# Optimization experiments

Hardware: AMD Instinct MI355X
Metric: run time of the kernel (lower is better)

Reference implementation:

```python
import jax, jax.numpy as jnp
import numpy as np
from jax.ops import segment_sum, segment_max

N_NODES = 10000
N_EDGES = 160000
N_GRAPHS = 32
IN_DIM = 128
HID = 256
HEADS = 4


def setup_inputs() -> dict:
    key = jax.random.key(0)
    ks = jax.random.split(key, 12)
    x = jax.random.normal(ks[0], (N_NODES, IN_DIM), dtype=jnp.float32)
    edge_index = jax.random.randint(ks[1], (2, N_EDGES), 0, N_NODES, dtype=jnp.int64)
    batch = jnp.sort(jax.random.randint(ks[2], (N_NODES,), 0, N_GRAPHS, dtype=jnp.int64))
    s = 0.05
    params = {
        "W1": jax.random.normal(ks[3], (IN_DIM, HID), dtype=jnp.float32) * s,
        "b1": jnp.zeros((HID,), dtype=jnp.float32),
        "W2": jax.random.normal(ks[4], (HID, HID), dtype=jnp.float32) * s,
        "b2": jnp.zeros((HID,), dtype=jnp.float32),
        "Wg": jax.random.normal(ks[5], (HID, HEADS * HID), dtype=jnp.float32) * s,
        "att_src": jax.random.normal(ks[6], (HEADS, HID), dtype=jnp.float32) * s,
        "att_dst": jax.random.normal(ks[7], (HEADS, HID), dtype=jnp.float32) * s,
        "bg": jnp.zeros((HID,), dtype=jnp.float32),
        "W_heads": jax.random.normal(ks[8], (HID, 4), dtype=jnp.float32) * s,
        "b_heads": jnp.zeros((4,), dtype=jnp.float32),
    }
    return {"x": x, "edge_index": edge_index, "batch": batch, **params}


def _add_self_loops(edge_index, n):
    loop = jnp.arange(n, dtype=edge_index.dtype)
    src = jnp.concatenate([edge_index[0], loop])
    dst = jnp.concatenate([edge_index[1], loop])
    return src, dst


def _gcn_conv(x, W, b, src, dst, n):
    # PyG GCNConv: add self-loops, symmetric normalization D^-1/2 A D^-1/2
    h = x @ W                                   # [N, out]
    deg = segment_sum(jnp.ones_like(src, dtype=h.dtype), dst, num_segments=n)
    dinv = jax.lax.rsqrt(jnp.maximum(deg, 1e-12))
    coef = dinv[src] * dinv[dst]                # [E+N]
    out = segment_sum(h[src] * coef[:, None], dst, num_segments=n)
    return out + b


def _gat_conv(x, Wg, att_src, att_dst, bg, src, dst, n):
    # PyG GATConv(heads=4, concat=False): mean over heads, leaky_relu slope 0.2
    h = (x @ Wg).reshape(n, HEADS, HID)         # [N, H, C]
    a_src = jnp.einsum('nhc,hc->nh', h, att_src)
    a_dst = jnp.einsum('nhc,hc->nh', h, att_dst)
    e = jax.nn.leaky_relu(a_src[src] + a_dst[dst], 0.2)   # [E+N, H]
    m = segment_max(e, dst, num_segments=n)
    e = jnp.exp(e - m[dst])
    z = segment_sum(e, dst, num_segments=n)
    alpha = e / (z[dst] + 1e-16)                # softmax over edges into each dst
    out = segment_sum(h[src] * alpha[:, :, None], dst, num_segments=n)  # [N, H, C]
    return out.mean(axis=1) + bg


def reference(x, edge_index, batch, W1, b1, W2, b2, Wg, att_src, att_dst, bg, W_heads, b_heads):
    n = x.shape[0]
    src, dst = _add_self_loops(edge_index, n)
    h1 = jax.nn.relu(_gcn_conv(x, W1, b1, src, dst, n))
    h2 = jax.nn.relu(_gcn_conv(h1, W2, b2, src, dst, n))
    h3 = jax.nn.relu(_gat_conv(h2, Wg, att_src, att_dst, bg, src, dst, n))
    # global_mean_pool
    ones = jnp.ones((n,), dtype=h3.dtype)
    cnt = segment_sum(ones, batch, num_segments=N_GRAPHS)
    pooled = segment_sum(h3, batch, num_segments=N_GRAPHS) / jnp.maximum(cnt, 1.0)[:, None]
    # four scalar heads stacked: cols = [energy_absorption, elastic_modulus, ballistic_limit, penetration_resistance]
    return pooled @ W_heads + b_heads           # [G, 4]
```

## Files before the change

### kernel.cpp

```cpp
#include <hip/hip_runtime.h>
#include <cmath>

#define IN_DIM 128
#define HID 256
#define NHEADS 4
#define NGRAPHS 32

typedef unsigned short u16;
typedef __attribute__((ext_vector_type(8))) short bfrag8;
typedef __attribute__((ext_vector_type(4))) float f32x4;

__device__ __forceinline__ u16 f2bf(float x) {
  unsigned u = __float_as_uint(x);
  unsigned r = (u + 0x7fffu + ((u >> 16) & 1u)) >> 16;
  return (u16)r;
}
__device__ __forceinline__ float bf2f(u16 v) {
  return __uint_as_float(((unsigned)v) << 16);
}
__device__ __forceinline__ float lof(unsigned u) { return __uint_as_float(u << 16); }
__device__ __forceinline__ float hif(unsigned u) { return __uint_as_float(u & 0xffff0000u); }
__device__ __forceinline__ float lrelu02(float x) { return x > 0.f ? x : 0.2f * x; }

#define GACC(U, W)                                                   \
  acc[0] += (W) * lof((U).x); acc[1] += (W) * hif((U).x);            \
  acc[2] += (W) * lof((U).y); acc[3] += (W) * hif((U).y);            \
  acc[4] += (W) * lof((U).z); acc[5] += (W) * hif((U).z);            \
  acc[6] += (W) * lof((U).w); acc[7] += (W) * hif((U).w);

#define GACC2(U, W)                                                  \
  a0 += (W) * lof((U).x); a1 += (W) * hif((U).x);                    \
  a2 += (W) * lof((U).y); a3 += (W) * hif((U).y);

__global__ __launch_bounds__(256) void count_edges_k(const int* __restrict__ dst,
                                                     int* __restrict__ cnt, int E) {
  int i = blockIdx.x * 256 + threadIdx.x;
  if (i < E) atomicAdd(&cnt[dst[i]], 1);
}

__global__ __launch_bounds__(256) void fill_csr_k(const int* __restrict__ src,
                                                  const int* __restrict__ dst,
                                                  const int* __restrict__ row_ptr,
                                                  int* __restrict__ cursor,
                                                  int* __restrict__ csr_src, int E) {
  int i = blockIdx.x * 256 + threadIdx.x;
  if (i < E) {
    int d = dst[i];
    int p = atomicAdd(&cursor[d], 1);
    csr_src[row_ptr[d] + p] = src[i];
  }
}

__device__ void scan_dev(const int* __restrict__ cnt, int* __restrict__ row_ptr,
                         float* __restrict__ dinv, int n) {
  __shared__ int s_w[4];
  __shared__ int s_off[4];
  __shared__ int s_tot;
  int tid = threadIdx.x, wv = tid >> 6, lane = tid & 63;
  int carry = 0;
  int nch = (n + 255) >> 8;
  for (int c = 0; c < nch; c++) {
    int i = (c << 8) + tid;
    int v = (i < n) ? cnt[i] : 0;
    int incl = v;
    #pragma unroll
    for (int off = 1; off < 64; off <<= 1) {
      int t = __shfl_up(incl, off);
      if (lane >= off) incl += t;
    }
    if (lane == 63) s_w[wv] = incl;
    __syncthreads();
    if (tid == 0) {
      int a0 = s_w[0], a1 = s_w[1], a2 = s_w[2], a3 = s_w[3];
      s_off[0] = 0; s_off[1] = a0; s_off[2] = a0 + a1; s_off[3] = a0 + a1 + a2;
      s_tot = a0 + a1 + a2 + a3;
    }
    __syncthreads();
    int excl = incl - v + s_off[wv] + carry;
    if (i < n) {
      row_ptr[i] = excl;
      dinv[i] = rsqrtf((float)(v + 1));
    }
    carry += s_tot;
    __syncthreads();
  }
  if (tid == 0) row_ptr[n] = carry;
}

__device__ void pack_a_dev(const float* __restrict__ A, u16* __restrict__ Ap,
                           int K, int KT, int wid, int lane) {
  int fm = wid / KT, kt = wid - fm * KT;
  int m = fm * 16 + (lane & 15);
  int kb = kt * 32 + (lane >> 4) * 8;
  const float* src = A + (size_t)m * K + kb;
  float4 v0 = *(const float4*)src;
  float4 v1 = *(const float4*)(src + 4);
  float vv[8] = {v0.x, v0.y, v0.z, v0.w, v1.x, v1.y, v1.z, v1.w};
  u16 hi[8], lo[8];
  #pragma unroll
  for (int j = 0; j < 8; j++) {
    u16 h = f2bf(vv[j]);
    hi[j] = h;
    lo[j] = f2bf(vv[j] - bf2f(h));
  }
  u16* dstp = Ap + ((size_t)fm * KT + kt) * 1024 + lane * 8;
  *(ushort4*)(dstp)       = make_ushort4(hi[0], hi[1], hi[2], hi[3]);
  *(ushort4*)(dstp + 4)   = make_ushort4(hi[4], hi[5], hi[6], hi[7]);
  *(ushort4*)(dstp + 512) = make_ushort4(lo[0], lo[1], lo[2], lo[3]);
  *(ushort4*)(dstp + 516) = make_ushort4(lo[4], lo[5], lo[6], lo[7]);
}

__device__ void pack_b_dev(const float* __restrict__ B, u16* __restrict__ Bp,
                           int N, int KT, int wid, int lane) {
  int fn = wid / KT, kt = wid - fn * KT;
  int n = fn * 16 + (lane & 15);
  int kb = kt * 32 + (lane >> 4) * 8;
  float vv[8];
  #pragma unroll
  for (int j = 0; j < 8; j++) vv[j] = B[(size_t)(kb + j) * N + n];
  u16 hi[8], lo[8];
  #pragma unroll
  for (int j = 0; j < 8; j++) {
    u16 h = f2bf(vv[j]);
    hi[j] = h;
    lo[j] = f2bf(vv[j] - bf2f(h));
  }
  u16* dstp = Bp + ((size_t)fn * KT + kt) * 1024 + lane * 8;
  *(ushort4*)(dstp)       = make_ushort4(hi[0], hi[1], hi[2], hi[3]);
  *(ushort4*)(dstp + 4)   = make_ushort4(hi[4], hi[5], hi[6], hi[7]);
  *(ushort4*)(dstp + 512) = make_ushort4(lo[0], lo[1], lo[2], lo[3]);
  *(ushort4*)(dstp + 516) = make_ushort4(lo[4], lo[5], lo[6], lo[7]);
}

__global__ __launch_bounds__(256) void prep_k(const float* __restrict__ x,
                                              const float* __restrict__ W1,
                                              const float* __restrict__ W2,
                                              const float* __restrict__ Wg,
                                              const float* __restrict__ att_src,
                                              const float* __restrict__ att_dst,
                                              const int* __restrict__ cnt,
                                              int* __restrict__ row_ptr,
                                              float* __restrict__ dinv,
                                              u16* __restrict__ xp,
                                              u16* __restrict__ w1p,
                                              u16* __restrict__ w2p,
                                              u16* __restrict__ wgp,
                                              float* __restrict__ w_s,
                                              float* __restrict__ w_d,
                                              int NFM, int N) {
  __shared__ float red_s[4][NHEADS];
  __shared__ float red_d[4][NHEADS];
  int b = blockIdx.x;
  int tid = threadIdx.x;
  int lane = tid & 63;
  if (b == 0) {
    scan_dev(cnt, row_ptr, dinv, N);
    return;
  }
  b -= 1;
  int XB = NFM;
  if (b < XB) {
    int wid = b * 4 + (tid >> 6);
    if (wid < NFM * 4) pack_a_dev(x, xp, IN_DIM, 4, wid, lane);
  } else if (b < XB + 16) {
    pack_b_dev(W1, w1p, HID, 4, (b - XB) * 4 + (tid >> 6), lane);
  } else if (b < XB + 48) {
    pack_b_dev(W2, w2p, HID, 8, (b - XB - 16) * 4 + (tid >> 6), lane);
  } else if (b < XB + 176) {
    pack_b_dev(Wg, wgp, NHEADS * HID, 8, (b - XB - 48) * 4 + (tid >> 6), lane);
  } else {
    int k = b - (XB + 176);
    int c = tid, wvv = c >> 6, ln = c & 63;
    #pragma unroll
    for (int h = 0; h < NHEADS; h++) {
      float w = Wg[(size_t)k * (NHEADS * HID) + h * HID + c];
      float vs = w * att_src[h * HID + c];
      float vd = w * att_dst[h * HID + c];
      #pragma unroll
      for (int off = 32; off; off >>= 1) {
        vs += __shfl_xor(vs, off);
        vd += __shfl_xor(vd, off);
      }
      if (ln == 0) { red_s[wvv][h] = vs; red_d[wvv][h] = vd; }
    }
    __syncthreads();
    if (c < NHEADS)
      w_s[k * NHEADS + c] = red_s[0][c] + red_s[1][c] + red_s[2][c] + red_s[3][c];
    else if (c < 2 * NHEADS) {
      int h = c - NHEADS;
      w_d[k * NHEADS + h] = red_d[0][h] + red_d[1][h] + red_d[2][h] + red_d[3][h];
    }
  }
}

template <int KT, int LDC, bool ALO>
__global__ __launch_bounds__(256) void mfma_gemm_k(const u16* __restrict__ Ap,
                                                   const u16* __restrict__ Bp,
                                                   u16* __restrict__ Cb, int M) {
  int tid = threadIdx.x;
  int w = tid >> 6, lane = tid & 63;
  int wm = w >> 1, wn = w & 1;
  int fm0 = blockIdx.y * 4 + wm * 2;
  int fn0 = blockIdx.x * 4 + wn * 2;
  f32x4 acc[2][2] = {};
  #pragma unroll
  for (int kt = 0; kt < KT; kt++) {
    bfrag8 a_hi[2], a_lo[2], b_hi[2], b_lo[2];
    #pragma unroll
    for (int f = 0; f < 2; f++) {
      const u16* pa = Ap + ((size_t)(fm0 + f) * KT + kt) * 1024 + lane * 8;
      a_hi[f] = *(const bfrag8*)pa;
      if constexpr (ALO) a_lo[f] = *(const bfrag8*)(pa + 512);
      const u16* pb = Bp + ((size_t)(fn0 + f) * KT + kt) * 1024 + lane * 8;
      b_hi[f] = *(const bfrag8*)pb;
      b_lo[f] = *(const bfrag8*)(pb + 512);
    }
    #pragma unroll
    for (int f = 0; f < 2; f++) {
      #pragma unroll
      for (int g = 0; g < 2; g++) {
        acc[f][g] = __builtin_amdgcn_mfma_f32_16x16x32_bf16(a_hi[f], b_hi[g], acc[f][g], 0, 0, 0);
        acc[f][g] = __builtin_amdgcn_mfma_f32_16x16x32_bf16(a_hi[f], b_lo[g], acc[f][g], 0, 0, 0);
        if constexpr (ALO)
          acc[f][g] = __builtin_amdgcn_mfma_f32_16x16x32_bf16(a_lo[f], b_hi[g], acc[f][g], 0, 0, 0);
      }
    }
  }
  int r0 = (lane >> 4) * 4;
  int cl = lane & 15;
  #pragma unroll
  for (int f = 0; f < 2; f++) {
    #pragma unroll
    for (int g = 0; g < 2; g++) {
      int col = (fn0 + g) * 16 + cl;
      #pragma unroll
      for (int r = 0; r < 4; r++) {
        int row = (fm0 + f) * 16 + r0 + r;
        if (row < M) Cb[(size_t)row * LDC + col] = f2bf(acc[f][g][r]);
      }
    }
  }
}

template <bool LOGITS, bool PACK_LO, bool SORT>
__global__ __launch_bounds__(256) void gcn_agg_k(const u16* __restrict__ t,
                                                 const int* __restrict__ row_ptr,
                                                 int* __restrict__ csr_src,
                                                 const float* __restrict__ dinv,
                                                 const float* __restrict__ bias,
                                                 u16* __restrict__ apack,
                                                 const float* __restrict__ w_s,
                                                 const float* __restrict__ w_d,
                                                 float4* __restrict__ a_src4,
                                                 float4* __restrict__ a_dst4, int N) {
  int wv = threadIdx.x >> 6, lane = threadIdx.x & 63;
  int i = blockIdx.x * 4 + wv;
  if (i >= N) return;
  float di = dinv[i];
  int c4 = lane * 4;
  int beg = row_ptr[i], end = row_ptr[i + 1];
  int deg = end - beg;
  float a0, a1, a2, a3;
  {
    uint2 u = *(const uint2*)&t[(size_t)i * HID + c4];
    float w = di * di;
    a0 = w * lof(u.x); a1 = w * hif(u.x); a2 = w * lof(u.y); a3 = w * hif(u.y);
  }
  if (deg <= 64) {
    int s = (lane < deg) ? csr_src[beg + lane] : 0x7fffffff;
    if constexpr (SORT) {
      if (deg > 1) {
        #pragma unroll
        for (int k = 2; k <= 64; k <<= 1) {
          #pragma unroll
          for (int j = k >> 1; j > 0; j >>= 1) {
            int vp = __shfl_xor(s, j);
            bool lower = ((lane & j) == 0);
            bool up = ((lane & k) == 0);
            int mn = min(s, vp), mx = max(s, vp);
            s = (lower == up) ? mn : mx;
          }
        }
        if (lane < deg) csr_src[beg + lane] = s;
      }
    }
    float w = (lane < deg) ? dinv[s] * di : 0.f;
    int e = 0;
    for (; e + 3 < deg; e += 4) {
      int s0 = __shfl(s, e), s1 = __shfl(s, e + 1);
      int s2 = __shfl(s, e + 2), s3 = __shfl(s, e + 3);
      float w0 = __shfl(w, e), w1 = __shfl(w, e + 1);
      float w2 = __shfl(w, e + 2), w3 = __shfl(w, e + 3);
      uint2 u0 = *(const uint2*)&t[(size_t)s0 * HID + c4];
      uint2 u1 = *(const uint2*)&t[(size_t)s1 * HID + c4];
      uint2 u2 = *(const uint2*)&t[(size_t)s2 * HID + c4];
      uint2 u3 = *(const uint2*)&t[(size_t)s3 * HID + c4];
      GACC2(u0, w0); GACC2(u1, w1); GACC2(u2, w2); GACC2(u3, w3);
    }
    for (; e < deg; e++) {
      int s0 = __shfl(s, e);
      float w0 = __shfl(w, e);
      uint2 u = *(const uint2*)&t[(size_t)s0 * HID + c4];
      GACC2(u, w0);
    }
  } else {
    int e = beg;
    for (; e + 3 < end; e += 4) {
      int s0 = csr_src[e + 0], s1 = csr_src[e + 1];
      int s2 = csr_src[e + 2], s3 = csr_src[e + 3];
      float w0 = dinv[s0] * di, w1 = dinv[s1] * di;
      float w2 = dinv[s2] * di, w3 = dinv[s3] * di;
      uint2 u0 = *(const uint2*)&t[(size_t)s0 * HID + c4];
      uint2 u1 = *(const uint2*)&t[(size_t)s1 * HID + c4];
      uint2 u2 = *(const uint2*)&t[(size_t)s2 * HID + c4];
      uint2 u3 = *(const uint2*)&t[(size_t)s3 * HID + c4];
      GACC2(u0, w0); GACC2(u1, w1); GACC2(u2, w2); GACC2(u3, w3);
    }
    for (; e < end; e++) {
      int s = csr_src[e];
      float w = dinv[s] * di;
      uint2 u = *(const uint2*)&t[(size_t)s * HID + c4];
      GACC2(u, w);
    }
  }
  float4 bv = *(const float4*)&bias[c4];
  float v0 = fmaxf(a0 + bv.x, 0.f), v1 = fmaxf(a1 + bv.y, 0.f);
  float v2 = fmaxf(a2 + bv.z, 0.f), v3 = fmaxf(a3 + bv.w, 0.f);
  {
    int fm = i >> 4, kt = c4 >> 5;
    int pl = (i & 15) + 16 * ((c4 >> 3) & 3);
    int j = c4 & 7;
    size_t base = ((size_t)fm * 8 + kt) * 1024 + pl * 8 + j;
    u16 h0 = f2bf(v0), h1 = f2bf(v1), h2 = f2bf(v2), h3 = f2bf(v3);
    *(ushort4*)&apack[base] = make_ushort4(h0, h1, h2, h3);
    if constexpr (PACK_LO)
      *(ushort4*)&apack[base + 512] =
          make_ushort4(f2bf(v0 - bf2f(h0)), f2bf(v1 - bf2f(h1)),
                       f2bf(v2 - bf2f(h2)), f2bf(v3 - bf2f(h3)));
  }
  if constexpr (LOGITS) {
    const float4* ws4 = (const float4*)w_s;
    const float4* wd4 = (const float4*)w_d;
    float4 s0 = ws4[c4 + 0], s1 = ws4[c4 + 1], s2 = ws4[c4 + 2], s3 = ws4[c4 + 3];
    float4 d0 = wd4[c4 + 0], d1 = wd4[c4 + 1], d2 = wd4[c4 + 2], d3 = wd4[c4 + 3];
    float ps0 = v0 * s0.x + v1 * s1.x + v2 * s2.x + v3 * s3.x;
    float ps1 = v0 * s0.y + v1 * s1.y + v2 * s2.y + v3 * s3.y;
    float ps2 = v0 * s0.z + v1 * s1.z + v2 * s2.z + v3 * s3.z;
    float ps3 = v0 * s0.w + v1 * s1.w + v2 * s2.w + v3 * s3.w;
    float pd0 = v0 * d0.x + v1 * d1.x + v2 * d2.x + v3 * d3.x;
    float pd1 = v0 * d0.y + v1 * d1.y + v2 * d2.y + v3 * d3.y;
    float pd2 = v0 * d0.z + v1 * d1.z + v2 * d2.z + v3 * d3.z;
    float pd3 = v0 * d0.w + v1 * d1.w + v2 * d2.w + v3 * d3.w;
    #pragma unroll
    for (int off = 32; off; off >>= 1) {
      ps0 += __shfl_xor(ps0, off); ps1 += __shfl_xor(ps1, off);
      ps2 += __shfl_xor(ps2, off); ps3 += __shfl_xor(ps3, off);
      pd0 += __shfl_xor(pd0, off); pd1 += __shfl_xor(pd1, off);
      pd2 += __shfl_xor(pd2, off); pd3 += __shfl_xor(pd3, off);
    }
    if (lane == 0) {
      a_src4[i] = make_float4(ps0, ps1, ps2, ps3);
      a_dst4[i] = make_float4(pd0, pd1, pd2, pd3);
    }
  }
}

__global__ __launch_bounds__(256) void gat_agg_k(const u16* __restrict__ hgT,
                                                 const int* __restrict__ row_ptr,
                                                 const int* __restrict__ csr_src,
                                                 const float4* __restrict__ a_src4,
                                                 const float4* __restrict__ a_dst4,
                                                 const float* __restrict__ bg,
                                                 float* __restrict__ out, int N) {
  __shared__ int s_src[4][64];
  __shared__ float s_al[4][2][64];
  __shared__ float s_comb[2][32][9];
  int wv = threadIdx.x >> 6, lane = threadIdx.x & 63;
  int nodeSlot = wv >> 1, half = wv & 1;
  int i = blockIdx.x * 2 + nodeSlot;
  if (i >= N) { __syncthreads(); return; }
  int beg = row_ptr[i], end = row_ptr[i + 1];
  int deg = end - beg;
  float4 ad = a_dst4[i];
  int hsel = lane >> 5;
  const u16* rowbase = hgT + half * 512 + lane * 8;
  float acc[8];
  #pragma unroll
  for (int j = 0; j < 8; j++) acc[j] = 0.f;

  if (deg <= 63) {
    int s = (lane < deg) ? csr_src[beg + lane] : i;
    bool valid = (lane <= deg);
    float4 as = a_src4[s];
    float l0 = valid ? lrelu02(as.x + ad.x) : -INFINITY;
    float l1 = valid ? lrelu02(as.y + ad.y) : -INFINITY;
    float l2 = valid ? lrelu02(as.z + ad.z) : -INFINITY;
    float l3 = valid ? lrelu02(as.w + ad.w) : -INFINITY;
    float m0 = l0, m1 = l1, m2 = l2, m3 = l3;
    #pragma unroll
    for (int off = 32; off; off >>= 1) {
      m0 = fmaxf(m0, __shfl_xor(m0, off)); m1 = fmaxf(m1, __shfl_xor(m1, off));
      m2 = fmaxf(m2, __shfl_xor(m2, off)); m3 = fmaxf(m3, __shfl_xor(m3, off));
    }
    float e0 = valid ? expf(l0 - m0) : 0.f;
    float e1 = valid ? expf(l1 - m1) : 0.f;
    float e2 = valid ? expf(l2 - m2) : 0.f;
    float e3 = valid ? expf(l3 - m3) : 0.f;
    float z0 = e0, z1 = e1, z2 = e2, z3 = e3;
    #pragma unroll
    for (int off = 32; off; off >>= 1) {
      z0 += __shfl_xor(z0, off); z1 += __shfl_xor(z1, off);
      z2 += __shfl_xor(z2, off); z3 += __shfl_xor(z3, off);
    }
    s_src[wv][lane] = s;
    if (half == 0) {
      s_al[wv][0][lane] = e0 / (z0 + 1e-16f);
      s_al[wv][1][lane] = e1 / (z1 + 1e-16f);
    } else {
      s_al[wv][0][lane] = e2 / (z2 + 1e-16f);
      s_al[wv][1][lane] = e3 / (z3 + 1e-16f);
    }
    int nk = deg + 1;
    int e = 0;
    for (; e + 3 < nk; e += 4) {
      int sa = s_src[wv][e + 0], sb = s_src[wv][e + 1];
      int sc = s_src[wv][e + 2], sd = s_src[wv][e + 3];
      float wa = s_al[wv][hsel][e + 0], wb = s_al[wv][hsel][e + 1];
      float wc = s_al[wv][hsel][e + 2], wd = s_al[wv][hsel][e + 3];
      uint4 ua = *(const uint4*)(rowbase + (size_t)sa * 1024);
      uint4 ub = *(const uint4*)(rowbase + (size_t)sb * 1024);
      uint4 uc = *(const uint4*)(rowbase + (size_t)sc * 1024);
      uint4 ud = *(const uint4*)(rowbase + (size_t)sd * 1024);
      GACC(ua, wa); GACC(ub, wb); GACC(uc, wc); GACC(ud, wd);
    }
    for (; e < nk; e++) {
      int sa = s_src[wv][e];
      float wa = s_al[wv][hsel][e];
      uint4 ua = *(const uint4*)(rowbase + (size_t)sa * 1024);
      GACC(ua, wa);
    }
  } else {
    float4 asi = a_src4[i];
    float ls0 = lrelu02(asi.x + ad.x), ls1 = lrelu02(asi.y + ad.y);
    float ls2 = lrelu02(asi.z + ad.z), ls3 = lrelu02(asi.w + ad.w);
    float m0 = ls0, m1 = ls1, m2 = ls2, m3 = ls3;
    for (int e = beg + lane; e < end; e += 64) {
      float4 as = a_src4[csr_src[e]];
      m0 = fmaxf(m0, lrelu02(as.x + ad.x)); m1 = fmaxf(m1, lrelu02(as.y + ad.y));
      m2 = fmaxf(m2, lrelu02(as.z + ad.z)); m3 = fmaxf(m3, lrelu02(as.w + ad.w));
    }
    #pragma unroll
    for (int off = 32; off; off >>= 1) {
      m0 = fmaxf(m0, __shfl_xor(m0, off)); m1 = fmaxf(m1, __shfl_xor(m1, off));
      m2 = fmaxf(m2, __shfl_xor(m2, off)); m3 = fmaxf(m3, __shfl_xor(m3, off));
    }
    float z0 = (lane == 0) ? expf(ls0 - m0) : 0.f;
    float z1 = (lane == 0) ? expf(ls1 - m1) : 0.f;
    float z2 = (lane == 0) ? expf(ls2 - m2) : 0.f;
    float z3 = (lane == 0) ? expf(ls3 - m3) : 0.f;
    for (int e = beg + lane; e < end; e += 64) {
      float4 as = a_src4[csr_src[e]];
      z0 += expf(lrelu02(as.x + ad.x) - m0); z1 += expf(lrelu02(as.y + ad.y) - m1);
      z2 += expf(lrelu02(as.z + ad.z) - m2); z3 += expf(lrelu02(as.w + ad.w) - m3);
    }
    #pragma unroll
    for (int off = 32; off; off >>= 1) {
      z0 += __shfl_xor(z0, off); z1 += __shfl_xor(z1, off);
      z2 += __shfl_xor(z2, off); z3 += __shfl_xor(z3, off);
    }
    float iz0 = 1.f / (z0 + 1e-16f), iz1 = 1.f / (z1 + 1e-16f);
    float iz2 = 1.f / (z2 + 1e-16f), iz3 = 1.f / (z3 + 1e-16f);
    {
      float w0 = expf(ls0 - m0) * iz0, w1 = expf(ls1 - m1) * iz1;
      float w2 = expf(ls2 - m2) * iz2, w3 = expf(ls3 - m3) * iz3;
      float aw = (half == 0) ? (hsel == 0 ? w0 : w1) : (hsel == 0 ? w2 : w3);
      uint4 u = *(const uint4*)(rowbase + (size_t)i * 1024);
      GACC(u, aw);
    }
    for (int base = beg; base < end; base += 64) {
      int mc = min(64, end - base);
      if (lane < mc) {
        int s = csr_src[base + lane];
        float4 as = a_src4[s];
        s_src[wv][lane] = s;
        if (half == 0) {
          s_al[wv][0][lane] = expf(lrelu02(as.x + ad.x) - m0) * iz0;
          s_al[wv][1][lane] = expf(lrelu02(as.y + ad.y) - m1) * iz1;
        } else {
          s_al[wv][0][lane] = expf(lrelu02(as.z + ad.z) - m2) * iz2;
          s_al[wv][1][lane] = expf(lrelu02(as.w + ad.w) - m3) * iz3;
        }
      }
      for (int e = 0; e < mc; e++) {
        int sa = s_src[wv][e];
        float wa = s_al[wv][hsel][e];
        uint4 ua = *(const uint4*)(rowbase + (size_t)sa * 1024);
        GACC(ua, wa);
      }
    }
  }
  #pragma unroll
  for (int j = 0; j < 8; j++) acc[j] += __shfl_xor(acc[j], 32);
  if (half == 1 && lane < 32) {
    #pragma unroll
    for (int j = 0; j < 8; j++) s_comb[nodeSlot][lane][j] = acc[j];
  }
  __syncthreads();
  if (half == 0 && lane < 32) {
    int cb = lane * 8;
    float o[8];
    #pragma unroll
    for (int j = 0; j < 8; j++)
      o[j] = fmaxf((acc[j] + s_comb[nodeSlot][lane][j]) * 0.25f + bg[cb + j], 0.f);
    float* op = out + (size_t)i * HID + cb;
    *(float4*)(op + 0) = make_float4(o[0], o[1], o[2], o[3]);
    *(float4*)(op + 4) = make_float4(o[4], o[5], o[6], o[7]);
  }
}

#define POOL_CHUNK 50
__global__ __launch_bounds__(256) void pool_acc_k(const float* __restrict__ h3,
                                                  const int* __restrict__ batch,
                                                  float* __restrict__ pooled,
                                                  float* __restrict__ gcnt, int N) {
  int c = threadIdx.x;
  int i0 = blockIdx.x * POOL_CHUNK;
  int i1 = min(i0 + POOL_CHUNK, N);
  if (i0 >= N) return;
  float acc = 0.f;
  int cur = batch[i0];
  int cnt_local = 0;
  for (int i = i0; i < i1; i++) {
    int g = batch[i];
    if (g != cur) {
      atomicAdd(&pooled[cur * HID + c], acc);
      if (c == 0) atomicAdd(&gcnt[cur], (float)cnt_local);
      acc = 0.f;
      cnt_local = 0;
      cur = g;
    }
    acc += h3[(size_t)i * HID + c];
    cnt_local++;
  }
  atomicAdd(&pooled[cur * HID + c], acc);
  if (c == 0) atomicAdd(&gcnt[cur], (float)cnt_local);
}

__global__ __launch_bounds__(128) void head_k(const float* __restrict__ pooled,
                                              const float* __restrict__ gcnt,
                                              const float* __restrict__ W_heads,
                                              const float* __restrict__ b_heads,
                                              float* __restrict__ out) {
  int tid = threadIdx.x;
  if (tid >= NGRAPHS * 4) return;
  int g = tid >> 2, k = tid & 3;
  float invc = 1.f / fmaxf(gcnt[g], 1.f);
  float acc = 0.f;
  for (int c = 0; c < HID; c++) acc += pooled[g * HID + c] * W_heads[c * 4 + k];
  out[g * 4 + k] = acc * invc + b_heads[k];
}

extern "C" void kernel_launch(void* const* d_in, const int* in_sizes, int n_in,
                              void* d_out, int out_size, void* d_ws, size_t ws_size,
                              hipStream_t stream) {
  const float* x = (const float*)d_in[0];
  const int* ei = (const int*)d_in[1];
  const int* batch = (const int*)d_in[2];
  const float* W1 = (const float*)d_in[3];
  const float* b1 = (const float*)d_in[4];
  const float* W2 = (const float*)d_in[5];
  const float* b2 = (const float*)d_in[6];
  const float* Wg = (const float*)d_in[7];
  const float* att_src = (const float*)d_in[8];
  const float* att_dst = (const float*)d_in[9];
  const float* bg = (const float*)d_in[10];
  const float* W_heads = (const float*)d_in[11];
  const float* b_heads = (const float*)d_in[12];
  float* out = (float*)d_out;

  const int N = in_sizes[0] / IN_DIM;
  const int E = in_sizes[1] / 2;
  const int* src = ei;
  const int* dst = ei + E;

  const int NFM = N / 16;
  const int NFMP = ((N + 63) / 64) * 4;

  char* ws = (char*)d_ws;
  size_t off = 0;
  auto take = [&](size_t bytes) -> char* {
    char* p = ws + off;
    off = (off + bytes + 255) & ~(size_t)255;
    return p;
  };
  int* cnt      = (int*)take((size_t)N * 4);
  int* cursor   = (int*)take((size_t)N * 4);
  float* pooled = (float*)take((size_t)NGRAPHS * HID * 4 + NGRAPHS * 4);
  float* gcnt   = pooled + NGRAPHS * HID;
  size_t zero_span = off;
  int* row_ptr  = (int*)take((size_t)(N + 1) * 4);
  int* csr_src  = (int*)take((size_t)E * 4);
  float* dinv   = (float*)take((size_t)N * 4);
  float4* a_src4 = (float4*)take((size_t)N * 16);
  float4* a_dst4 = (float4*)take((size_t)N * 16);
  float* w_s    = (float*)take((size_t)HID * NHEADS * 4);
  float* w_d    = (float*)take((size_t)HID * NHEADS * 4);
  u16*   tb     = (u16*)take((size_t)N * HID * 2);
  float* h3     = (float*)take((size_t)N * HID * 4);
  u16*   hgT    = (u16*)take((size_t)N * NHEADS * HID * 2);
  u16*   xp     = (u16*)take((size_t)NFMP * 4 * 1024 * 2);
  u16*   h1p    = (u16*)take((size_t)NFMP * 8 * 1024 * 2);
  u16*   h2p    = (u16*)take((size_t)NFMP * 8 * 1024 * 2);
  u16*   w1p    = (u16*)take((size_t)16 * 4 * 1024 * 2);
  u16*   w2p    = (u16*)take((size_t)16 * 8 * 1024 * 2);
  u16*   wgp    = (u16*)take((size_t)64 * 8 * 1024 * 2);

  hipMemsetAsync(cnt, 0, zero_span, stream);

  int eb = (E + 255) / 256;
  count_edges_k<<<eb, 256, 0, stream>>>(dst, cnt, E);
  prep_k<<<1 + NFM + 176 + 256, 256, 0, stream>>>(x, W1, W2, Wg, att_src, att_dst,
                                                  cnt, row_ptr, dinv,
                                                  xp, w1p, w2p, wgp, w_s, w_d, NFM, N);
  fill_csr_k<<<eb, 256, 0, stream>>>(src, dst, row_ptr, cursor, csr_src, E);

  int mg64 = (N + 63) / 64;
  int ng4 = (N + 3) / 4;
  int ng2 = (N + 1) / 2;
  mfma_gemm_k<4, HID, true><<<dim3(4, mg64), 256, 0, stream>>>(xp, w1p, tb, N);
  gcn_agg_k<false, true, true><<<ng4, 256, 0, stream>>>(tb, row_ptr, csr_src, dinv, b1,
                                                        h1p, nullptr, nullptr, nullptr, nullptr, N);
  mfma_gemm_k<8, HID, true><<<dim3(4, mg64), 256, 0, stream>>>(h1p, w2p, tb, N);
  gcn_agg_k<true, false, false><<<ng4, 256, 0, stream>>>(tb, row_ptr, csr_src, dinv, b2,
                                                         h2p, w_s, w_d, a_src4, a_dst4, N);
  mfma_gemm_k<8, NHEADS * HID, false><<<dim3(16, mg64), 256, 0, stream>>>(h2p, wgp, hgT, N);
  gat_agg_k<<<ng2, 256, 0, stream>>>(hgT, row_ptr, csr_src, a_src4, a_dst4, bg, h3, N);
  int pb = (N + POOL_CHUNK - 1) / POOL_CHUNK;
  pool_acc_k<<<pb, 256, 0, stream>>>(h3, batch, pooled, gcnt, N);
  head_k<<<1, 128, 0, stream>>>(pooled, gcnt, W_heads, b_heads, out);
}
```

Before: 205.2 us.

## Remap GEMM blocks per XCD, drop in-kernel neighbor sort, widen GAT gather unroll

The GEMM launch becomes a 1D grid whose block ids are remapped so that all column tiles of a row tile land on the same XCD, improving L2 reuse of A rows. The bitonic sort of each node's neighbor list in the first GCN aggregation is removed, which saves shuffles and a write-back but gives up the locality that sorted gathers had. The GAT aggregation gather loop is unrolled to 8 outstanding 16-byte loads to raise memory-level parallelism at the cost of more registers.

```diff
diff --git a/kernel.cpp b/kernel.cpp
--- a/kernel.cpp
+++ b/kernel.cpp
@@ -193,15 +193,22 @@
   }
 }
 
-template <int KT, int LDC, bool ALO>
+template <int KT, int LDC, bool ALO, int GX>
 __global__ __launch_bounds__(256) void mfma_gemm_k(const u16* __restrict__ Ap,
                                                    const u16* __restrict__ Bp,
-                                                   u16* __restrict__ Cb, int M) {
+                                                   u16* __restrict__ Cb,
+                                                   int M, int MY) {
+  int bid = blockIdx.x;
+  int xcd = bid & 7;
+  int j = bid >> 3;
+  int by = xcd + 8 * (j / GX);
+  int bx = j - (j / GX) * GX;
+  if (by >= MY) return;
   int tid = threadIdx.x;
   int w = tid >> 6, lane = tid & 63;
   int wm = w >> 1, wn = w & 1;
-  int fm0 = blockIdx.y * 4 + wm * 2;
-  int fn0 = blockIdx.x * 4 + wn * 2;
+  int fm0 = by * 4 + wm * 2;
+  int fn0 = bx * 4 + wn * 2;
   f32x4 acc[2][2] = {};
   #pragma unroll
   for (int kt = 0; kt < KT; kt++) {
@@ -242,10 +249,10 @@
   }
 }
 
-template <bool LOGITS, bool PACK_LO, bool SORT>
+template <bool LOGITS, bool PACK_LO>
 __global__ __launch_bounds__(256) void gcn_agg_k(const u16* __restrict__ t,
                                                  const int* __restrict__ row_ptr,
-                                                 int* __restrict__ csr_src,
+                                                 const int* __restrict__ csr_src,
                                                  const float* __restrict__ dinv,
                                                  const float* __restrict__ bias,
                                                  u16* __restrict__ apack,
@@ -267,23 +274,7 @@
     a0 = w * lof(u.x); a1 = w * hif(u.x); a2 = w * lof(u.y); a3 = w * hif(u.y);
   }
   if (deg <= 64) {
-    int s = (lane < deg) ? csr_src[beg + lane] : 0x7fffffff;
-    if constexpr (SORT) {
-      if (deg > 1) {
-        #pragma unroll
-        for (int k = 2; k <= 64; k <<= 1) {
-          #pragma unroll
-          for (int j = k >> 1; j > 0; j >>= 1) {
-            int vp = __shfl_xor(s, j);
-            bool lower = ((lane & j) == 0);
-            bool up = ((lane & k) == 0);
-            int mn = min(s, vp), mx = max(s, vp);
-            s = (lower == up) ? mn : mx;
-          }
-        }
-        if (lane < deg) csr_src[beg + lane] = s;
-      }
-    }
+    int s = (lane < deg) ? csr_src[beg + lane] : 0;
     float w = (lane < deg) ? dinv[s] * di : 0.f;
     int e = 0;
     for (; e + 3 < deg; e += 4) {
@@ -422,16 +413,20 @@
     }
     int nk = deg + 1;
     int e = 0;
-    for (; e + 3 < nk; e += 4) {
-      int sa = s_src[wv][e + 0], sb = s_src[wv][e + 1];
-      int sc = s_src[wv][e + 2], sd = s_src[wv][e + 3];
-      float wa = s_al[wv][hsel][e + 0], wb = s_al[wv][hsel][e + 1];
-      float wc = s_al[wv][hsel][e + 2], wd = s_al[wv][hsel][e + 3];
-      uint4 ua = *(const uint4*)(rowbase + (size_t)sa * 1024);
-      uint4 ub = *(const uint4*)(rowbase + (size_t)sb * 1024);
-      uint4 uc = *(const uint4*)(rowbase + (size_t)sc * 1024);
-      uint4 ud = *(const uint4*)(rowbase + (size_t)sd * 1024);
-      GACC(ua, wa); GACC(ub, wb); GACC(uc, wc); GACC(ud, wd);
+    for (; e + 7 < nk; e += 8) {
+      int sv[8];
+      float wvv[8];
+      #pragma unroll
+      for (int q = 0; q < 8; q++) {
+        sv[q] = s_src[wv][e + q];
+        wvv[q] = s_al[wv][hsel][e + q];
+      }
+      uint4 u[8];
+      #pragma unroll
+      for (int q = 0; q < 8; q++)
+        u[q] = *(const uint4*)(rowbase + (size_t)sv[q] * 1024);
+      #pragma unroll
+      for (int q = 0; q < 8; q++) { GACC(u[q], wvv[q]); }
     }
     for (; e < nk; e++) {
       int sa = s_src[wv][e];
@@ -624,16 +619,18 @@
                                                   xp, w1p, w2p, wgp, w_s, w_d, NFM, N);
   fill_csr_k<<<eb, 256, 0, stream>>>(src, dst, row_ptr, cursor, csr_src, E);
 
-  int mg64 = (N + 63) / 64;
+  const int MY = (N + 63) / 64;
+  const int gemm_blks4 = 8 * ((MY + 7) / 8) * 4;
+  const int gemm_blks16 = 8 * ((MY + 7) / 8) * 16;
   int ng4 = (N + 3) / 4;
   int ng2 = (N + 1) / 2;
-  mfma_gemm_k<4, HID, true><<<dim3(4, mg64), 256, 0, stream>>>(xp, w1p, tb, N);
-  gcn_agg_k<false, true, true><<<ng4, 256, 0, stream>>>(tb, row_ptr, csr_src, dinv, b1,
-                                                        h1p, nullptr, nullptr, nullptr, nullptr, N);
-  mfma_gemm_k<8, HID, true><<<dim3(4, mg64), 256, 0, stream>>>(h1p, w2p, tb, N);
-  gcn_agg_k<true, false, false><<<ng4, 256, 0, stream>>>(tb, row_ptr, csr_src, dinv, b2,
-                                                         h2p, w_s, w_d, a_src4, a_dst4, N);
-  mfma_gemm_k<8, NHEADS * HID, false><<<dim3(16, mg64), 256, 0, stream>>>(h2p, wgp, hgT, N);
+  mfma_gemm_k<4, HID, true, 4><<<gemm_blks4, 256, 0, stream>>>(xp, w1p, tb, N, MY);
+  gcn_agg_k<false, true><<<ng4, 256, 0, stream>>>(tb, row_ptr, csr_src, dinv, b1,
+                                                  h1p, nullptr, nullptr, nullptr, nullptr, N);
+  mfma_gemm_k<8, HID, true, 4><<<gemm_blks4, 256, 0, stream>>>(h1p, w2p, tb, N, MY);
+  gcn_agg_k<true, false><<<ng4, 256, 0, stream>>>(tb, row_ptr, csr_src, dinv, b2,
+                                                  h2p, w_s, w_d, a_src4, a_dst4, N);
+  mfma_gemm_k<8, NHEADS * HID, false, 16><<<gemm_blks16, 256, 0, stream>>>(h2p, wgp, hgT, N, MY);
   gat_agg_k<<<ng2, 256, 0, stream>>>(hgT, row_ptr, csr_src, a_src4, a_dst4, bg, h3, N);
   int pb = (N + POOL_CHUNK - 1) / POOL_CHUNK;
   pool_acc_k<<<pb, 256, 0, stream>>>(h3, batch, pooled, gcnt, N);
```

Measured after the change: 210.9 us. 2.8% more time.

## Fuse mean-pool with regression heads and drop in-wave CSR sort

Applied to the files above, without the earlier changes.

Global mean pooling and the four regression heads are merged into one kernel. Each block binary-searches its graph's node range in the sorted batch array, sums one strided part of the rows, and applies W_heads before atomically adding into the zeroed output. This removes a launch and the pooled scratch buffer, at the cost of an extra memset of the output. Separately, the GCN aggregation loses its shuffle-based small-degree path and the bitonic sort of CSR sources, so neighbour order stays as fill_csr produced it and gather locality may get worse.

```diff
diff --git a/kernel.cpp b/kernel.cpp
--- a/kernel.cpp
+++ b/kernel.cpp
@@ -242,10 +242,10 @@
   }
 }
 
-template <bool LOGITS, bool PACK_LO, bool SORT>
+template <bool LOGITS, bool PACK_LO>
 __global__ __launch_bounds__(256) void gcn_agg_k(const u16* __restrict__ t,
                                                  const int* __restrict__ row_ptr,
-                                                 int* __restrict__ csr_src,
+                                                 const int* __restrict__ csr_src,
                                                  const float* __restrict__ dinv,
                                                  const float* __restrict__ bias,
                                                  u16* __restrict__ apack,
@@ -259,69 +259,29 @@
   float di = dinv[i];
   int c4 = lane * 4;
   int beg = row_ptr[i], end = row_ptr[i + 1];
-  int deg = end - beg;
   float a0, a1, a2, a3;
   {
     uint2 u = *(const uint2*)&t[(size_t)i * HID + c4];
     float w = di * di;
     a0 = w * lof(u.x); a1 = w * hif(u.x); a2 = w * lof(u.y); a3 = w * hif(u.y);
   }
-  if (deg <= 64) {
-    int s = (lane < deg) ? csr_src[beg + lane] : 0x7fffffff;
-    if constexpr (SORT) {
-      if (deg > 1) {
-        #pragma unroll
-        for (int k = 2; k <= 64; k <<= 1) {
-          #pragma unroll
-          for (int j = k >> 1; j > 0; j >>= 1) {
-            int vp = __shfl_xor(s, j);
-            bool lower = ((lane & j) == 0);
-            bool up = ((lane & k) == 0);
-            int mn = min(s, vp), mx = max(s, vp);
-            s = (lower == up) ? mn : mx;
-          }
-        }
-        if (lane < deg) csr_src[beg + lane] = s;
-      }
-    }
-    float w = (lane < deg) ? dinv[s] * di : 0.f;
-    int e = 0;
-    for (; e + 3 < deg; e += 4) {
-      int s0 = __shfl(s, e), s1 = __shfl(s, e + 1);
-      int s2 = __shfl(s, e + 2), s3 = __shfl(s, e + 3);
-      float w0 = __shfl(w, e), w1 = __shfl(w, e + 1);
-      float w2 = __shfl(w, e + 2), w3 = __shfl(w, e + 3);
-      uint2 u0 = *(const uint2*)&t[(size_t)s0 * HID + c4];
-      uint2 u1 = *(const uint2*)&t[(size_t)s1 * HID + c4];
-      uint2 u2 = *(const uint2*)&t[(size_t)s2 * HID + c4];
-      uint2 u3 = *(const uint2*)&t[(size_t)s3 * HID + c4];
-      GACC2(u0, w0); GACC2(u1, w1); GACC2(u2, w2); GACC2(u3, w3);
-    }
-    for (; e < deg; e++) {
-      int s0 = __shfl(s, e);
-      float w0 = __shfl(w, e);
-      uint2 u = *(const uint2*)&t[(size_t)s0 * HID + c4];
-      GACC2(u, w0);
-    }
-  } else {
-    int e = beg;
-    for (; e + 3 < end; e += 4) {
-      int s0 = csr_src[e + 0], s1 = csr_src[e + 1];
-      int s2 = csr_src[e + 2], s3 = csr_src[e + 3];
-      float w0 = dinv[s0] * di, w1 = dinv[s1] * di;
-      float w2 = dinv[s2] * di, w3 = dinv[s3] * di;
-      uint2 u0 = *(const uint2*)&t[(size_t)s0 * HID + c4];
-      uint2 u1 = *(const uint2*)&t[(size_t)s1 * HID + c4];
-      uint2 u2 = *(const uint2*)&t[(size_t)s2 * HID + c4];
-      uint2 u3 = *(const uint2*)&t[(size_t)s3 * HID + c4];
-      GACC2(u0, w0); GACC2(u1, w1); GACC2(u2, w2); GACC2(u3, w3);
-    }
-    for (; e < end; e++) {
-      int s = csr_src[e];
-      float w = dinv[s] * di;
-      uint2 u = *(const uint2*)&t[(size_t)s * HID + c4];
-      GACC2(u, w);
-    }
+  int e = beg;
+  for (; e + 3 < end; e += 4) {
+    int s0 = csr_src[e + 0], s1 = csr_src[e + 1];
+    int s2 = csr_src[e + 2], s3 = csr_src[e + 3];
+    float w0 = dinv[s0] * di, w1 = dinv[s1] * di;
+    float w2 = dinv[s2] * di, w3 = dinv[s3] * di;
+    uint2 u0 = *(const uint2*)&t[(size_t)s0 * HID + c4];
+    uint2 u1 = *(const uint2*)&t[(size_t)s1 * HID + c4];
+    uint2 u2 = *(const uint2*)&t[(size_t)s2 * HID + c4];
+    uint2 u3 = *(const uint2*)&t[(size_t)s3 * HID + c4];
+    GACC2(u0, w0); GACC2(u1, w1); GACC2(u2, w2); GACC2(u3, w3);
+  }
+  for (; e < end; e++) {
+    int s = csr_src[e];
+    float w = dinv[s] * di;
+    uint2 u = *(const uint2*)&t[(size_t)s * HID + c4];
+    GACC2(u, w);
   }
   float4 bv = *(const float4*)&bias[c4];
   float v0 = fmaxf(a0 + bv.x, 0.f), v1 = fmaxf(a1 + bv.y, 0.f);
@@ -518,46 +478,50 @@
   }
 }
 
-#define POOL_CHUNK 50
-__global__ __launch_bounds__(256) void pool_acc_k(const float* __restrict__ h3,
-                                                  const int* __restrict__ batch,
-                                                  float* __restrict__ pooled,
-                                                  float* __restrict__ gcnt, int N) {
+__global__ __launch_bounds__(256) void pool_head_k(const float* __restrict__ h3,
+                                                   const int* __restrict__ batch,
+                                                   const float* __restrict__ W_heads,
+                                                   const float* __restrict__ b_heads,
+                                                   float* __restrict__ out, int N) {
+  int g = blockIdx.x >> 3;
+  int part = blockIdx.x & 7;
   int c = threadIdx.x;
-  int i0 = blockIdx.x * POOL_CHUNK;
-  int i1 = min(i0 + POOL_CHUNK, N);
-  if (i0 >= N) return;
-  float acc = 0.f;
-  int cur = batch[i0];
-  int cnt_local = 0;
-  for (int i = i0; i < i1; i++) {
-    int g = batch[i];
-    if (g != cur) {
-      atomicAdd(&pooled[cur * HID + c], acc);
-      if (c == 0) atomicAdd(&gcnt[cur], (float)cnt_local);
-      acc = 0.f;
-      cnt_local = 0;
-      cur = g;
-    }
-    acc += h3[(size_t)i * HID + c];
-    cnt_local++;
-  }
-  atomicAdd(&pooled[cur * HID + c], acc);
-  if (c == 0) atomicAdd(&gcnt[cur], (float)cnt_local);
-}
-
-__global__ __launch_bounds__(128) void head_k(const float* __restrict__ pooled,
-                                              const float* __restrict__ gcnt,
-                                              const float* __restrict__ W_heads,
-                                              const float* __restrict__ b_heads,
-                                              float* __restrict__ out) {
-  int tid = threadIdx.x;
-  if (tid >= NGRAPHS * 4) return;
-  int g = tid >> 2, k = tid & 3;
-  float invc = 1.f / fmaxf(gcnt[g], 1.f);
-  float acc = 0.f;
-  for (int c = 0; c < HID; c++) acc += pooled[g * HID + c] * W_heads[c * 4 + k];
-  out[g * 4 + k] = acc * invc + b_heads[k];
+  __shared__ int s_bounds[2];
+  if (c < 2) {
+    int target = g + c;
+    int lo = 0, hi = N;
+    while (lo < hi) {
+      int mid = (lo + hi) >> 1;
+      if (batch[mid] < target) lo = mid + 1; else hi = mid;
+    }
+    s_bounds[c] = lo;
+  }
+  __syncthreads();
+  int i0 = s_bounds[0], i1 = s_bounds[1];
+  float acc0 = 0.f, acc1 = 0.f;
+  int i = i0 + part;
+  for (; i + 8 < i1; i += 16) {
+    acc0 += h3[(size_t)i * HID + c];
+    acc1 += h3[(size_t)(i + 8) * HID + c];
+  }
+  if (i < i1) acc0 += h3[(size_t)i * HID + c];
+  float acc = acc0 + acc1;
+  float invc = 1.f / fmaxf((float)(i1 - i0), 1.f);
+  float4 wh = *(const float4*)&W_heads[c * 4];
+  float p0 = acc * wh.x, p1 = acc * wh.y, p2 = acc * wh.z, p3 = acc * wh.w;
+  int lane = c & 63, wv = c >> 6;
+  #pragma unroll
+  for (int off = 32; off; off >>= 1) {
+    p0 += __shfl_xor(p0, off); p1 += __shfl_xor(p1, off);
+    p2 += __shfl_xor(p2, off); p3 += __shfl_xor(p3, off);
+  }
+  __shared__ float s_red[4][4];
+  if (lane == 0) { s_red[wv][0] = p0; s_red[wv][1] = p1; s_red[wv][2] = p2; s_red[wv][3] = p3; }
+  __syncthreads();
+  if (c < 4) {
+    float r = s_red[0][c] + s_red[1][c] + s_red[2][c] + s_red[3][c];
+    atomicAdd(&out[g * 4 + c], r * invc + b_heads[c] * 0.125f);
+  }
 }
 
 extern "C" void kernel_launch(void* const* d_in, const int* in_sizes, int n_in,
@@ -595,8 +559,6 @@
   };
   int* cnt      = (int*)take((size_t)N * 4);
   int* cursor   = (int*)take((size_t)N * 4);
-  float* pooled = (float*)take((size_t)NGRAPHS * HID * 4 + NGRAPHS * 4);
-  float* gcnt   = pooled + NGRAPHS * HID;
   size_t zero_span = off;
   int* row_ptr  = (int*)take((size_t)(N + 1) * 4);
   int* csr_src  = (int*)take((size_t)E * 4);
@@ -616,6 +578,7 @@
   u16*   wgp    = (u16*)take((size_t)64 * 8 * 1024 * 2);
 
   hipMemsetAsync(cnt, 0, zero_span, stream);
+  hipMemsetAsync(out, 0, (size_t)out_size * 4, stream);
 
   int eb = (E + 255) / 256;
   count_edges_k<<<eb, 256, 0, stream>>>(dst, cnt, E);
@@ -628,14 +591,12 @@
   int ng4 = (N + 3) / 4;
   int ng2 = (N + 1) / 2;
   mfma_gemm_k<4, HID, true><<<dim3(4, mg64), 256, 0, stream>>>(xp, w1p, tb, N);
-  gcn_agg_k<false, true, true><<<ng4, 256, 0, stream>>>(tb, row_ptr, csr_src, dinv, b1,
-                                                        h1p, nullptr, nullptr, nullptr, nullptr, N);
+  gcn_agg_k<false, true><<<ng4, 256, 0, stream>>>(tb, row_ptr, csr_src, dinv, b1,
+                                                  h1p, nullptr, nullptr, nullptr, nullptr, N);
   mfma_gemm_k<8, HID, true><<<dim3(4, mg64), 256, 0, stream>>>(h1p, w2p, tb, N);
-  gcn_agg_k<true, false, false><<<ng4, 256, 0, stream>>>(tb, row_ptr, csr_src, dinv, b2,
-                                                         h2p, w_s, w_d, a_src4, a_dst4, N);
+  gcn_agg_k<true, false><<<ng4, 256, 0, stream>>>(tb, row_ptr, csr_src, dinv, b2,
+                                                  h2p, w_s, w_d, a_src4, a_dst4, N);
   mfma_gemm_k<8, NHEADS * HID, false><<<dim3(16, mg64), 256, 0, stream>>>(h2p, wgp, hgT, N);
   gat_agg_k<<<ng2, 256, 0, stream>>>(hgT, row_ptr, csr_src, a_src4, a_dst4, bg, h3, N);
-  int pb = (N + POOL_CHUNK - 1) / POOL_CHUNK;
-  pool_acc_k<<<pb, 256, 0, stream>>>(h3, batch, pooled, gcnt, N);
-  head_k<<<1, 128, 0, stream>>>(pooled, gcnt, W_heads, b_heads, out);
-}
+  pool_head_k<<<NGRAPHS * 8, 256, 0, stream>>>(h3, batch, W_heads, b_heads, out, N);
+}
```

Result: faster. 197.9 us (-3.6%).
